# Kernel tuning notes

Measured on AMD Instinct MI355X. Metric: run time of the kernel, lower is better.

## Reference

```python
import jax, jax.numpy as jnp
import numpy as np

N_NODES = 50000
N_EDGES = 800000
N_REL = 3
N_GRAPHS = 500
EMB = 128
IN_DIM = EMB * 3
HID = 256
N_CLASS = 10
N_SHAPE, N_COLOR, MAX_POS = 8, 8, 128


def rgcn_layer(h, src, dst, etype, W, root, b):
    """PyG RGCNConv with default aggr='mean':
    out[v] = sum_r mean_{(j->v) in E_r} h[j] @ W[r] + h[v] @ root + b
    Aggregate raw features per (dst, relation) bucket, then apply relation matmuls.
    """
    N, R = h.shape[0], W.shape[0]
    seg = dst * R + etype  # combined (node, relation) segment id
    sums = jax.ops.segment_sum(h[src], seg, num_segments=N * R)          # (N*R, d)
    cnt = jax.ops.segment_sum(jnp.ones(seg.shape, h.dtype), seg, num_segments=N * R)
    mean = (sums / jnp.maximum(cnt, 1.0)[:, None]).reshape(N, R, -1)     # (N, R, d)
    return jnp.einsum('nrd,rdh->nh', mean, W) + h @ root + b


def setup_inputs() -> dict:
    key = jax.random.key(0)
    ks = jax.random.split(key, 20)
    f32 = jnp.float32
    inp = {
        's': jax.random.randint(ks[0], (N_NODES,), 0, N_SHAPE),
        'c': jax.random.randint(ks[1], (N_NODES,), 0, N_COLOR),
        'p': jax.random.randint(ks[2], (N_NODES,), 0, MAX_POS),
        'edge_index': jax.random.randint(ks[3], (2, N_EDGES), 0, N_NODES),
        'edge_type': jax.random.randint(ks[4], (N_EDGES,), 0, N_REL),
        'batch': jnp.sort(jax.random.randint(ks[5], (N_NODES,), 0, N_GRAPHS)),
        'shape_emb': jax.random.normal(ks[6], (N_SHAPE, EMB), f32),
        'color_emb': jax.random.normal(ks[7], (N_COLOR, EMB), f32),
        'pos_emb': jax.random.normal(ks[8], (MAX_POS, EMB), f32),
        'W1': jax.random.normal(ks[9], (N_REL, IN_DIM, HID), f32) / np.sqrt(IN_DIM),
        'root1': jax.random.normal(ks[10], (IN_DIM, HID), f32) / np.sqrt(IN_DIM),
        'b1': jnp.zeros((HID,), f32),
        'W2': jax.random.normal(ks[11], (N_REL, HID, HID), f32) / np.sqrt(HID),
        'root2': jax.random.normal(ks[12], (HID, HID), f32) / np.sqrt(HID),
        'b2': jnp.zeros((HID,), f32),
        'lin_w': jax.random.normal(ks[13], (HID, N_CLASS), f32) / np.sqrt(HID),
        'lin_b': jnp.zeros((N_CLASS,), f32),
    }
    return inp


def reference(s, c, p, edge_index, edge_type, batch,
              shape_emb, color_emb, pos_emb,
              W1, root1, b1, W2, root2, b2, lin_w, lin_b):
    src, dst = edge_index[0], edge_index[1]
    h = jnp.concatenate([shape_emb[s], color_emb[c], pos_emb[p]], axis=-1)  # (N, 3*emb)
    h = jax.nn.relu(rgcn_layer(h, src, dst, edge_type, W1, root1, b1))
    h = jax.nn.relu(rgcn_layer(h, src, dst, edge_type, W2, root2, b2))
    # global_mean_pool over graphs
    gsum = jax.ops.segment_sum(h, batch, num_segments=N_GRAPHS)
    gcnt = jax.ops.segment_sum(jnp.ones((h.shape[0],), h.dtype), batch, num_segments=N_GRAPHS)
    pooled = gsum / jnp.maximum(gcnt, 1.0)[:, None]
    return pooled @ lin_w + lin_b
```

## Files before the change

### kernel.cpp

```cpp
#include <hip/hip_runtime.h>
#include <hip/hip_bf16.h>

#define NN 50000
#define NE 800000
#define NR 3
#define NG 500
#define NB (NN * NR)
#define NCLS 10
#define NCMB 8192
#define CHUNK 2048
#define NBLK ((NB + CHUNK - 1) / CHUNK)

typedef __hip_bfloat16 bf16;
typedef __attribute__((ext_vector_type(8))) short short8;
typedef __attribute__((ext_vector_type(4))) float floatx4;

static __device__ __forceinline__ float b2f(bf16 x) { return __bfloat162float(x); }
static __device__ __forceinline__ bf16  f2b(float x) { return __float2bfloat16(x); }
static __device__ __forceinline__ float bs2f(short x) {
    return __bfloat162float(*reinterpret_cast<const bf16*>(&x));
}
static __device__ __forceinline__ short f2bs(float x) {
    bf16 b = __float2bfloat16(x);
    return *reinterpret_cast<const short*>(&b);
}

__global__ __launch_bounds__(256) void zero_u32(unsigned* __restrict__ p, long n) {
    long i = (long)blockIdx.x * 256 + threadIdx.x;
    if (i < n) p[i] = 0u;
}

__global__ __launch_bounds__(256) void count_edges(const int* __restrict__ ei,
                                                   const int* __restrict__ et,
                                                   int* __restrict__ cnt) {
    int e = blockIdx.x * 256 + threadIdx.x;
    if (e >= NE) return;
    atomicAdd(&cnt[ei[NE + e] * NR + et[e]], 1);
}

__global__ __launch_bounds__(256) void scan_block_sums(const int* __restrict__ cnt,
                                                       int* __restrict__ bsum) {
    __shared__ int sm[256];
    int b = blockIdx.x, t = threadIdx.x;
    int base = b * CHUNK + t * 8, s = 0;
#pragma unroll
    for (int j = 0; j < 8; ++j) { int i = base + j; if (i < NB) s += cnt[i]; }
    sm[t] = s; __syncthreads();
    for (int st = 128; st; st >>= 1) { if (t < st) sm[t] += sm[t + st]; __syncthreads(); }
    if (!t) bsum[b] = sm[0];
}

__global__ void scan_base(const int* __restrict__ bsum, int* __restrict__ bbase,
                          int* __restrict__ off) {
    if (threadIdx.x == 0 && blockIdx.x == 0) {
        int run = 0;
        for (int i = 0; i < NBLK; ++i) { bbase[i] = run; run += bsum[i]; }
        off[NB] = run;
    }
}

__global__ __launch_bounds__(256) void scan_write(const int* __restrict__ cnt,
                                                  const int* __restrict__ bbase,
                                                  int* __restrict__ off,
                                                  int* __restrict__ cursor) {
    int b = blockIdx.x, t = threadIdx.x;
    int base = b * CHUNK + t * 8;
    int v[8], ts = 0;
#pragma unroll
    for (int j = 0; j < 8; ++j) { int i = base + j; v[j] = (i < NB) ? cnt[i] : 0; ts += v[j]; }
    int lane = t & 63, wv = t >> 6;
    int incl = ts;
    for (int d = 1; d < 64; d <<= 1) {
        int o = __shfl_up(incl, d, 64);
        if (lane >= d) incl += o;
    }
    __shared__ int wsum[4];
    if (lane == 63) wsum[wv] = incl;
    __syncthreads();
    int wbase = 0;
    for (int w = 0; w < wv; ++w) wbase += wsum[w];
    int run = bbase[b] + wbase + incl - ts;
#pragma unroll
    for (int j = 0; j < 8; ++j) {
        int i = base + j;
        if (i < NB) { off[i] = run; cursor[i] = run; }
        run += v[j];
    }
}

__global__ __launch_bounds__(256) void scatter_edges(const int* __restrict__ ei,
                                                     const int* __restrict__ et,
                                                     const int* __restrict__ combo,
                                                     int* __restrict__ cursor,
                                                     int* __restrict__ eidx,
                                                     int* __restrict__ ecmb) {
    int e = blockIdx.x * 256 + threadIdx.x;
    if (e >= NE) return;
    int b = ei[NE + e] * NR + et[e];
    int pos = atomicAdd(&cursor[b], 1);
    int s = ei[e];
    eidx[pos] = s;
    ecmb[pos] = combo[s];
}

__global__ __launch_bounds__(256) void tab_gemm(const float* __restrict__ se,
                                                const float* __restrict__ ce,
                                                const float* __restrict__ pe,
                                                const float* __restrict__ W1,
                                                const float* __restrict__ root1,
                                                float* __restrict__ tab) {
    int bid = blockIdx.x;
    int r = bid / 144, row = bid % 144;
    int t = threadIdx.x;
    const float* A; int segk;
    if (row < 8)       { A = se + row * 128;        segk = 0; }
    else if (row < 16) { A = ce + (row - 8) * 128;  segk = 128; }
    else               { A = pe + (row - 16) * 128; segk = 256; }
    const float* W = (r < 3) ? (W1 + (size_t)r * 384 * 256) : root1;
    float acc = 0.f;
    for (int k = 0; k < 128; ++k)
        acc += A[k] * W[(size_t)(segk + k) * 256 + t];
    tab[((size_t)r * 144 + row) * 256 + t] = acc;
}

__global__ __launch_bounds__(256) void node_combo(const int* __restrict__ s,
                                                  const int* __restrict__ c,
                                                  const int* __restrict__ p,
                                                  int* __restrict__ combo) {
    int n = blockIdx.x * 256 + threadIdx.x;
    if (n < NN) combo[n] = (s[n] << 10) | (c[n] << 7) | p[n];
}

__global__ __launch_bounds__(256) void comb_build(const float* __restrict__ tab,
                                                  const float* __restrict__ b1,
                                                  bf16* __restrict__ comb) {
    int bid = blockIdx.x;
    int r = bid >> 13, cmb = bid & (NCMB - 1);
    int d = threadIdx.x;
    int si = cmb >> 10, ci = (cmb >> 7) & 7, pi = cmb & 127;
    const float* tr = tab + (size_t)r * 144 * 256;
    float v = tr[si * 256 + d] + tr[(8 + ci) * 256 + d] + tr[(16 + pi) * 256 + d];
    if (r == 3) v += b1[d];
    comb[(size_t)bid * 256 + d] = f2b(v);
}

__global__ __launch_bounds__(256) void l1_fused(const int* __restrict__ off,
                                                const int* __restrict__ ecmb,
                                                const int* __restrict__ combo,
                                                const bf16* __restrict__ comb,
                                                bf16* __restrict__ h1) {
    int wave = threadIdx.x >> 6, lane = threadIdx.x & 63;
    int dst = blockIdx.x * 4 + wave;
    if (dst >= NN) return;
    int half = lane >> 5, li8 = (lane & 31) * 8;
    float acc[8];
    if (half == 0) {
        int cmbD = combo[dst];
        short8 rv = *(const short8*)(comb + ((size_t)(3 * NCMB) + cmbD) * 256 + li8);
#pragma unroll
        for (int i = 0; i < 8; ++i) acc[i] = bs2f(rv[i]);
    } else {
#pragma unroll
        for (int i = 0; i < 8; ++i) acc[i] = 0.f;
    }
    for (int r = 0; r < NR; ++r) {
        int lo = off[dst * NR + r], hi = off[dst * NR + r + 1];
        if (hi <= lo) continue;
        const bf16* cr = comb + (size_t)r * NCMB * 256;
        float s[8] = {};
        int j = lo;
        for (; j + 8 <= hi; j += 8) {
            int c0 = ecmb[j + half],     c1 = ecmb[j + 2 + half];
            int c2 = ecmb[j + 4 + half], c3 = ecmb[j + 6 + half];
            short8 v0 = *(const short8*)(cr + (size_t)c0 * 256 + li8);
            short8 v1 = *(const short8*)(cr + (size_t)c1 * 256 + li8);
            short8 v2 = *(const short8*)(cr + (size_t)c2 * 256 + li8);
            short8 v3 = *(const short8*)(cr + (size_t)c3 * 256 + li8);
#pragma unroll
            for (int i = 0; i < 8; ++i)
                s[i] += (bs2f(v0[i]) + bs2f(v1[i])) + (bs2f(v2[i]) + bs2f(v3[i]));
        }
        for (; j + 2 <= hi; j += 2) {
            int c0 = ecmb[j + half];
            short8 v0 = *(const short8*)(cr + (size_t)c0 * 256 + li8);
#pragma unroll
            for (int i = 0; i < 8; ++i) s[i] += bs2f(v0[i]);
        }
        if (j < hi && half == 0) {
            short8 v0 = *(const short8*)(cr + (size_t)ecmb[j] * 256 + li8);
#pragma unroll
            for (int i = 0; i < 8; ++i) s[i] += bs2f(v0[i]);
        }
        float inv = 1.0f / (float)(hi - lo);
#pragma unroll
        for (int i = 0; i < 8; ++i) {
            float tot = s[i] + __shfl_xor(s[i], 32);
            if (half == 0) acc[i] += tot * inv;
        }
    }
    if (half == 0) {
        short8 o;
#pragma unroll
        for (int i = 0; i < 8; ++i) o[i] = f2bs(fmaxf(acc[i], 0.f));
        *(short8*)(h1 + (size_t)dst * 256 + li8) = o;
    }
}

__global__ __launch_bounds__(256) void agg_all(const int* __restrict__ off,
                                               const int* __restrict__ eidx,
                                               const bf16* __restrict__ h1,
                                               bf16* __restrict__ hagg) {
    int wave = threadIdx.x >> 6, lane = threadIdx.x & 63;
    int dst = blockIdx.x * 4 + wave;
    if (dst >= NN) return;
    int half = lane >> 5, li8 = (lane & 31) * 8;
    for (int r = 0; r < NR; ++r) {
        int lo = off[dst * NR + r], hi = off[dst * NR + r + 1];
        float s[8] = {};
        int j = lo;
        for (; j + 8 <= hi; j += 8) {
            int e0 = eidx[j + half],     e1 = eidx[j + 2 + half];
            int e2 = eidx[j + 4 + half], e3 = eidx[j + 6 + half];
            short8 v0 = *(const short8*)(h1 + (size_t)e0 * 256 + li8);
            short8 v1 = *(const short8*)(h1 + (size_t)e1 * 256 + li8);
            short8 v2 = *(const short8*)(h1 + (size_t)e2 * 256 + li8);
            short8 v3 = *(const short8*)(h1 + (size_t)e3 * 256 + li8);
#pragma unroll
            for (int i = 0; i < 8; ++i)
                s[i] += (bs2f(v0[i]) + bs2f(v1[i])) + (bs2f(v2[i]) + bs2f(v3[i]));
        }
        for (; j + 2 <= hi; j += 2) {
            int e0 = eidx[j + half];
            short8 v0 = *(const short8*)(h1 + (size_t)e0 * 256 + li8);
#pragma unroll
            for (int i = 0; i < 8; ++i) s[i] += bs2f(v0[i]);
        }
        if (j < hi && half == 0) {
            short8 v0 = *(const short8*)(h1 + (size_t)eidx[j] * 256 + li8);
#pragma unroll
            for (int i = 0; i < 8; ++i) s[i] += bs2f(v0[i]);
        }
        float inv = (hi > lo) ? 1.0f / (float)(hi - lo) : 0.f;
        short8 o;
#pragma unroll
        for (int i = 0; i < 8; ++i) {
            float tot = s[i] + __shfl_xor(s[i], 32);
            o[i] = f2bs(tot * inv);
        }
        if (half == 0)
            *(short8*)(hagg + (size_t)dst * 768 + r * 256 + li8) = o;
    }
}

__global__ __launch_bounds__(256) void conv_w2cat(const float* __restrict__ W2,
                                                  const float* __restrict__ root2,
                                                  bf16* __restrict__ Wf) {
    int idx = blockIdx.x * 256 + threadIdx.x;
    if (idx >= 256 * 1024) return;
    int j     = idx & 7;
    int lane  = (idx >> 3) & 63;
    int ni    = (idx >> 9) & 3;
    int chunk = (idx >> 11) & 31;
    int colblk = idx >> 16;
    int col = colblk * 64 + ni * 16 + (lane & 15);
    int k   = chunk * 32 + (lane >> 4) * 8 + j;
    float v = (k < 768) ? W2[((size_t)(k >> 8) * 256 + (k & 255)) * 256 + col]
                        : root2[(size_t)(k - 768) * 256 + col];
    Wf[idx] = f2b(v);
}

__global__ __launch_bounds__(256) void gemm_cat(const bf16* __restrict__ hagg,
                                                const bf16* __restrict__ h1,
                                                const bf16* __restrict__ Wf,
                                                const float* __restrict__ bias,
                                                bf16* __restrict__ h2) {
    __shared__ short lds[4][32 * 40];
    const int t = threadIdx.x;
    const int wave = t >> 6, lane = t & 63;
    const int quad = lane >> 4, l16 = lane & 15;
    const int row0 = blockIdx.y * 64 + (wave & 1) * 32;
    const int colblk = blockIdx.x * 2 + (wave >> 1);
    const int rsub = lane >> 2;
    const int ksub = (lane & 3) * 8;
    short* A = lds[wave];

    const int r0 = min(row0 + rsub, NN - 1);
    const int r1 = min(row0 + 16 + rsub, NN - 1);
    const bf16* gA0 = hagg + (size_t)r0 * 768 + ksub;
    const bf16* gA1 = hagg + (size_t)r1 * 768 + ksub;
    const bf16* gH0 = h1 + (size_t)r0 * 256 + ksub;
    const bf16* gH1 = h1 + (size_t)r1 * 256 + ksub;
    const short8* bbase = (const short8*)Wf + (size_t)colblk * 32 * 4 * 64 + lane;

    auto loadA2 = [&](int k0, short8& a0, short8& a1) {
        if (k0 < 768) { a0 = *(const short8*)(gA0 + k0); a1 = *(const short8*)(gA1 + k0); }
        else          { a0 = *(const short8*)(gH0 + k0 - 768); a1 = *(const short8*)(gH1 + k0 - 768); }
    };
    auto loadB = [&](int chunk, short8* bf4) {
        const short8* bp = bbase + (size_t)chunk * 4 * 64;
#pragma unroll
        for (int ni = 0; ni < 4; ++ni) bf4[ni] = bp[ni * 64];
    };

    floatx4 acc[2][4] = {};
    short8 aC0, aC1, bC[4], aN0, aN1, bN[4];
    loadA2(0, aC0, aC1);
    loadB(0, bC);

    for (int i = 0; i < 32; ++i) {
        *(short8*)&A[rsub * 40 + ksub] = aC0;
        *(short8*)&A[(16 + rsub) * 40 + ksub] = aC1;
        if (i + 1 < 32) {
            loadA2((i + 1) * 32, aN0, aN1);
            loadB(i + 1, bN);
        }
        short8 af0 = *(const short8*)&A[l16 * 40 + quad * 8];
        short8 af1 = *(const short8*)&A[(16 + l16) * 40 + quad * 8];
#pragma unroll
        for (int ni = 0; ni < 4; ++ni) {
            acc[0][ni] = __builtin_amdgcn_mfma_f32_16x16x32_bf16(af0, bC[ni], acc[0][ni], 0, 0, 0);
            acc[1][ni] = __builtin_amdgcn_mfma_f32_16x16x32_bf16(af1, bC[ni], acc[1][ni], 0, 0, 0);
        }
        aC0 = aN0; aC1 = aN1;
#pragma unroll
        for (int ni = 0; ni < 4; ++ni) bC[ni] = bN[ni];
    }

#pragma unroll
    for (int mi = 0; mi < 2; ++mi) {
#pragma unroll
        for (int ni = 0; ni < 4; ++ni) {
            int n = colblk * 64 + ni * 16 + l16;
            float bn = bias[n];
#pragma unroll
            for (int ii = 0; ii < 4; ++ii) {
                int gm = row0 + mi * 16 + quad * 4 + ii;
                if (gm < NN) {
                    float v = acc[mi][ni][ii] + bn;
                    h2[(size_t)gm * 256 + n] = f2b(fmaxf(v, 0.f));
                }
            }
        }
    }
}

#define PN 64
__global__ __launch_bounds__(256) void pool_rle(const int* __restrict__ batch,
                                                const bf16* __restrict__ H,
                                                float* __restrict__ pool,
                                                float* __restrict__ gcnt) {
    int t = threadIdx.x;
    int n0 = blockIdx.x * PN;
    int nend = n0 + PN; if (nend > NN) nend = NN;
    int curg = batch[n0];
    float acc = 0.f, cnt = 0.f;
    for (int n = n0; n < nend; ++n) {
        int g = batch[n];
        if (g != curg) {
            atomicAdd(&pool[(size_t)curg * 256 + t], acc);
            if (t == 0) atomicAdd(&gcnt[curg], cnt);
            acc = 0.f; cnt = 0.f; curg = g;
        }
        acc += b2f(H[(size_t)n * 256 + t]);
        cnt += 1.f;
    }
    atomicAdd(&pool[(size_t)curg * 256 + t], acc);
    if (t == 0) atomicAdd(&gcnt[curg], cnt);
}

__global__ __launch_bounds__(256) void final_head(const float* __restrict__ pool,
                                                  const float* __restrict__ gcnt,
                                                  const float* __restrict__ lin_w,
                                                  const float* __restrict__ lin_b,
                                                  float* __restrict__ out) {
    __shared__ float sm[256];
    int g = blockIdx.x, t = threadIdx.x;
    float inv = 1.0f / fmaxf(gcnt[g], 1.0f);
    sm[t] = pool[(size_t)g * 256 + t] * inv;
    __syncthreads();
    if (t < NCLS) {
        float s = lin_b[t];
        for (int d = 0; d < 256; ++d) s += sm[d] * lin_w[d * NCLS + t];
        out[g * NCLS + t] = s;
    }
}

extern "C" void kernel_launch(void* const* d_in, const int* in_sizes, int n_in,
                              void* d_out, int out_size, void* d_ws, size_t ws_size,
                              hipStream_t stream) {
    const int*   s_idx = (const int*)d_in[0];
    const int*   c_idx = (const int*)d_in[1];
    const int*   p_idx = (const int*)d_in[2];
    const int*   ei    = (const int*)d_in[3];
    const int*   et    = (const int*)d_in[4];
    const int*   batch = (const int*)d_in[5];
    const float* se    = (const float*)d_in[6];
    const float* ce    = (const float*)d_in[7];
    const float* pe    = (const float*)d_in[8];
    const float* W1    = (const float*)d_in[9];
    const float* root1 = (const float*)d_in[10];
    const float* b1    = (const float*)d_in[11];
    const float* W2    = (const float*)d_in[12];
    const float* root2 = (const float*)d_in[13];
    const float* b2    = (const float*)d_in[14];
    const float* lin_w = (const float*)d_in[15];
    const float* lin_b = (const float*)d_in[16];
    float* out = (float*)d_out;

    char* w = (char*)d_ws;
    size_t o = 0;
    auto alloc = [&](size_t bytes) -> void* {
        o = (o + 15) & ~(size_t)15;
        void* ptr = w + o;
        o += bytes;
        return ptr;
    };
    bf16*  hagg   = (bf16*) alloc((size_t)NN * 768 * 2);
    bf16*  h1     = (bf16*) alloc((size_t)NN * 256 * 2);
    bf16*  h2     = (bf16*) alloc((size_t)NN * 256 * 2);
    bf16*  comb   = (bf16*) alloc((size_t)4 * NCMB * 256 * 2);
    int*   combo  = (int*)  alloc((size_t)NN * 4);
    int*   eidx   = (int*)  alloc((size_t)NE * 4);
    int*   ecmb   = (int*)  alloc((size_t)NE * 4);
    int*   cnt    = (int*)  alloc((size_t)NB * 4);
    int*   off    = (int*)  alloc((size_t)(NB + 1) * 4);
    int*   cursor = (int*)  alloc((size_t)NB * 4);
    int*   bsum   = (int*)  alloc((size_t)NBLK * 4);
    int*   bbase  = (int*)  alloc((size_t)NBLK * 4);
    float* tab    = (float*)alloc((size_t)4 * 144 * 256 * 4);
    bf16*  Wf     = (bf16*) alloc((size_t)256 * 1024 * 2);
    float* pool   = (float*)alloc((size_t)NG * 256 * 4);
    float* gcnt   = (float*)alloc((size_t)NG * 4);
    (void)ws_size;

    node_combo<<<(NN + 255) / 256, 256, 0, stream>>>(s_idx, c_idx, p_idx, combo);
    zero_u32<<<(NB + 255) / 256, 256, 0, stream>>>((unsigned*)cnt, NB);
    count_edges<<<(NE + 255) / 256, 256, 0, stream>>>(ei, et, cnt);
    scan_block_sums<<<NBLK, 256, 0, stream>>>(cnt, bsum);
    scan_base<<<1, 64, 0, stream>>>(bsum, bbase, off);
    scan_write<<<NBLK, 256, 0, stream>>>(cnt, bbase, off, cursor);
    scatter_edges<<<(NE + 255) / 256, 256, 0, stream>>>(ei, et, combo, cursor, eidx, ecmb);

    tab_gemm<<<4 * 144, 256, 0, stream>>>(se, ce, pe, W1, root1, tab);
    comb_build<<<4 * NCMB, 256, 0, stream>>>(tab, b1, comb);
    conv_w2cat<<<(256 * 1024 + 255) / 256, 256, 0, stream>>>(W2, root2, Wf);

    l1_fused<<<(NN + 3) / 4, 256, 0, stream>>>(off, ecmb, combo, comb, h1);

    agg_all<<<(NN + 3) / 4, 256, 0, stream>>>(off, eidx, h1, hagg);
    dim3 g2(2, (NN + 63) / 64);
    gemm_cat<<<g2, 256, 0, stream>>>(hagg, h1, Wf, b2, h2);

    zero_u32<<<(NG * 256 + NG + 255) / 256, 256, 0, stream>>>((unsigned*)pool, NG * 256 + NG);
    pool_rle<<<(NN + PN - 1) / PN, 256, 0, stream>>>(batch, h2, pool, gcnt);
    final_head<<<NG, 256, 0, stream>>>(pool, gcnt, lin_w, lin_b, out);
}
```

Before: 434.9 us.

## Merge prep kernels, fold scan base into scan_write, double-buffer gemm LDS

Independent setup kernels (combo, zeroing, table GEMM, W2 conversion) are merged into one launch, and the edge counting and comb table build into a second. The single-thread scan_base kernel is removed: each scan_write block now sums the preceding block totals itself. The gemm_cat main loop gets two LDS buffers and two register sets so global loads for the next step overlap the MFMAs on the current one. Together these cut launch count and serialization, at the cost of a small redundant prefix sum per block and higher register and LDS use in the GEMM.

```diff
diff --git a/kernel.cpp b/kernel.cpp
--- a/kernel.cpp
+++ b/kernel.cpp
@@ -11,6 +11,16 @@
 #define CHUNK 2048
 #define NBLK ((NB + CHUNK - 1) / CHUNK)
 
+#define P1_COMBO   196
+#define P1_ZCNT    586
+#define P1_ZPOOL   502
+#define P1_TAB     576
+#define P1_WF      1024
+#define P1_TOTAL   (P1_COMBO + P1_ZCNT + P1_ZPOOL + P1_TAB + P1_WF)
+#define P2_CNT     3125
+#define P2_COMB    (4 * NCMB)
+#define P2_TOTAL   (P2_CNT + P2_COMB)
+
 typedef __hip_bfloat16 bf16;
 typedef __attribute__((ext_vector_type(8))) short short8;
 typedef __attribute__((ext_vector_type(4))) float floatx4;
@@ -25,17 +35,90 @@
     return *reinterpret_cast<const short*>(&b);
 }
 
-__global__ __launch_bounds__(256) void zero_u32(unsigned* __restrict__ p, long n) {
-    long i = (long)blockIdx.x * 256 + threadIdx.x;
-    if (i < n) p[i] = 0u;
-}
-
-__global__ __launch_bounds__(256) void count_edges(const int* __restrict__ ei,
-                                                   const int* __restrict__ et,
-                                                   int* __restrict__ cnt) {
-    int e = blockIdx.x * 256 + threadIdx.x;
-    if (e >= NE) return;
-    atomicAdd(&cnt[ei[NE + e] * NR + et[e]], 1);
+__global__ __launch_bounds__(256) void prep1(const int* __restrict__ s,
+                                             const int* __restrict__ c,
+                                             const int* __restrict__ p,
+                                             const float* __restrict__ se,
+                                             const float* __restrict__ ce,
+                                             const float* __restrict__ pe,
+                                             const float* __restrict__ W1,
+                                             const float* __restrict__ root1,
+                                             const float* __restrict__ W2,
+                                             const float* __restrict__ root2,
+                                             int* __restrict__ combo,
+                                             unsigned* __restrict__ cnt,
+                                             unsigned* __restrict__ poolz,
+                                             float* __restrict__ tab,
+                                             bf16* __restrict__ Wf) {
+    int b = blockIdx.x, t = threadIdx.x;
+    if (b < P1_COMBO) {
+        int n = b * 256 + t;
+        if (n < NN) combo[n] = (s[n] << 10) | (c[n] << 7) | p[n];
+        return;
+    }
+    b -= P1_COMBO;
+    if (b < P1_ZCNT) {
+        int i = b * 256 + t;
+        if (i < NB) cnt[i] = 0u;
+        return;
+    }
+    b -= P1_ZCNT;
+    if (b < P1_ZPOOL) {
+        int i = b * 256 + t;
+        if (i < NG * 256 + NG) poolz[i] = 0u;
+        return;
+    }
+    b -= P1_ZPOOL;
+    if (b < P1_TAB) {
+        int r = b / 144, row = b % 144;
+        const float* A; int segk;
+        if (row < 8)       { A = se + row * 128;        segk = 0; }
+        else if (row < 16) { A = ce + (row - 8) * 128;  segk = 128; }
+        else               { A = pe + (row - 16) * 128; segk = 256; }
+        const float* W = (r < 3) ? (W1 + (size_t)r * 384 * 256) : root1;
+        float acc = 0.f;
+        for (int k = 0; k < 128; ++k)
+            acc += A[k] * W[(size_t)(segk + k) * 256 + t];
+        tab[((size_t)r * 144 + row) * 256 + t] = acc;
+        return;
+    }
+    b -= P1_TAB;
+    {
+        int idx = b * 256 + t;
+        int j     = idx & 7;
+        int lane  = (idx >> 3) & 63;
+        int ni    = (idx >> 9) & 3;
+        int chunk = (idx >> 11) & 31;
+        int colblk = idx >> 16;
+        int col = colblk * 64 + ni * 16 + (lane & 15);
+        int k   = chunk * 32 + (lane >> 4) * 8 + j;
+        float v = (k < 768) ? W2[((size_t)(k >> 8) * 256 + (k & 255)) * 256 + col]
+                            : root2[(size_t)(k - 768) * 256 + col];
+        Wf[idx] = f2b(v);
+    }
+}
+
+__global__ __launch_bounds__(256) void prep2(const int* __restrict__ ei,
+                                             const int* __restrict__ et,
+                                             int* __restrict__ cnt,
+                                             const float* __restrict__ tab,
+                                             const float* __restrict__ b1,
+                                             bf16* __restrict__ comb) {
+    int b = blockIdx.x, t = threadIdx.x;
+    if (b < P2_CNT) {
+        int e = b * 256 + t;
+        if (e < NE) atomicAdd(&cnt[ei[NE + e] * NR + et[e]], 1);
+        return;
+    }
+    b -= P2_CNT;
+    {
+        int r = b >> 13, cmb = b & (NCMB - 1);
+        int si = cmb >> 10, ci = (cmb >> 7) & 7, pi = cmb & 127;
+        const float* tr = tab + (size_t)r * 144 * 256;
+        float v = tr[si * 256 + t] + tr[(8 + ci) * 256 + t] + tr[(16 + pi) * 256 + t];
+        if (r == 3) v += b1[t];
+        comb[(size_t)b * 256 + t] = f2b(v);
+    }
 }
 
 __global__ __launch_bounds__(256) void scan_block_sums(const int* __restrict__ cnt,
@@ -50,20 +133,18 @@
     if (!t) bsum[b] = sm[0];
 }
 
-__global__ void scan_base(const int* __restrict__ bsum, int* __restrict__ bbase,
-                          int* __restrict__ off) {
-    if (threadIdx.x == 0 && blockIdx.x == 0) {
-        int run = 0;
-        for (int i = 0; i < NBLK; ++i) { bbase[i] = run; run += bsum[i]; }
-        off[NB] = run;
-    }
-}
-
 __global__ __launch_bounds__(256) void scan_write(const int* __restrict__ cnt,
-                                                  const int* __restrict__ bbase,
+                                                  const int* __restrict__ bsum,
                                                   int* __restrict__ off,
                                                   int* __restrict__ cursor) {
     int b = blockIdx.x, t = threadIdx.x;
+    int bbase = 0;
+    for (int i = 0; i < b; ++i) bbase += bsum[i];
+    if (b == 0 && t == 0) {
+        int tot = 0;
+        for (int i = 0; i < NBLK; ++i) tot += bsum[i];
+        off[NB] = tot;
+    }
     int base = b * CHUNK + t * 8;
     int v[8], ts = 0;
 #pragma unroll
@@ -79,7 +160,7 @@
     __syncthreads();
     int wbase = 0;
     for (int w = 0; w < wv; ++w) wbase += wsum[w];
-    int run = bbase[b] + wbase + incl - ts;
+    int run = bbase + wbase + incl - ts;
 #pragma unroll
     for (int j = 0; j < 8; ++j) {
         int i = base + j;
@@ -101,47 +182,6 @@
     int s = ei[e];
     eidx[pos] = s;
     ecmb[pos] = combo[s];
-}
-
-__global__ __launch_bounds__(256) void tab_gemm(const float* __restrict__ se,
-                                                const float* __restrict__ ce,
-                                                const float* __restrict__ pe,
-                                                const float* __restrict__ W1,
-                                                const float* __restrict__ root1,
-                                                float* __restrict__ tab) {
-    int bid = blockIdx.x;
-    int r = bid / 144, row = bid % 144;
-    int t = threadIdx.x;
-    const float* A; int segk;
-    if (row < 8)       { A = se + row * 128;        segk = 0; }
-    else if (row < 16) { A = ce + (row - 8) * 128;  segk = 128; }
-    else               { A = pe + (row - 16) * 128; segk = 256; }
-    const float* W = (r < 3) ? (W1 + (size_t)r * 384 * 256) : root1;
-    float acc = 0.f;
-    for (int k = 0; k < 128; ++k)
-        acc += A[k] * W[(size_t)(segk + k) * 256 + t];
-    tab[((size_t)r * 144 + row) * 256 + t] = acc;
-}
-
-__global__ __launch_bounds__(256) void node_combo(const int* __restrict__ s,
-                                                  const int* __restrict__ c,
-                                                  const int* __restrict__ p,
-                                                  int* __restrict__ combo) {
-    int n = blockIdx.x * 256 + threadIdx.x;
-    if (n < NN) combo[n] = (s[n] << 10) | (c[n] << 7) | p[n];
-}
-
-__global__ __launch_bounds__(256) void comb_build(const float* __restrict__ tab,
-                                                  const float* __restrict__ b1,
-                                                  bf16* __restrict__ comb) {
-    int bid = blockIdx.x;
-    int r = bid >> 13, cmb = bid & (NCMB - 1);
-    int d = threadIdx.x;
-    int si = cmb >> 10, ci = (cmb >> 7) & 7, pi = cmb & 127;
-    const float* tr = tab + (size_t)r * 144 * 256;
-    float v = tr[si * 256 + d] + tr[(8 + ci) * 256 + d] + tr[(16 + pi) * 256 + d];
-    if (r == 3) v += b1[d];
-    comb[(size_t)bid * 256 + d] = f2b(v);
 }
 
 __global__ __launch_bounds__(256) void l1_fused(const int* __restrict__ off,
@@ -252,29 +292,12 @@
     }
 }
 
-__global__ __launch_bounds__(256) void conv_w2cat(const float* __restrict__ W2,
-                                                  const float* __restrict__ root2,
-                                                  bf16* __restrict__ Wf) {
-    int idx = blockIdx.x * 256 + threadIdx.x;
-    if (idx >= 256 * 1024) return;
-    int j     = idx & 7;
-    int lane  = (idx >> 3) & 63;
-    int ni    = (idx >> 9) & 3;
-    int chunk = (idx >> 11) & 31;
-    int colblk = idx >> 16;
-    int col = colblk * 64 + ni * 16 + (lane & 15);
-    int k   = chunk * 32 + (lane >> 4) * 8 + j;
-    float v = (k < 768) ? W2[((size_t)(k >> 8) * 256 + (k & 255)) * 256 + col]
-                        : root2[(size_t)(k - 768) * 256 + col];
-    Wf[idx] = f2b(v);
-}
-
 __global__ __launch_bounds__(256) void gemm_cat(const bf16* __restrict__ hagg,
                                                 const bf16* __restrict__ h1,
                                                 const bf16* __restrict__ Wf,
                                                 const float* __restrict__ bias,
                                                 bf16* __restrict__ h2) {
-    __shared__ short lds[4][32 * 40];
+    __shared__ short lds[4][2][32 * 40];
     const int t = threadIdx.x;
     const int wave = t >> 6, lane = t & 63;
     const int quad = lane >> 4, l16 = lane & 15;
@@ -282,7 +305,8 @@
     const int colblk = blockIdx.x * 2 + (wave >> 1);
     const int rsub = lane >> 2;
     const int ksub = (lane & 3) * 8;
-    short* A = lds[wave];
+    short* A0 = lds[wave][0];
+    short* A1 = lds[wave][1];
 
     const int r0 = min(row0 + rsub, NN - 1);
     const int r1 = min(row0 + 16 + rsub, NN - 1);
@@ -303,27 +327,37 @@
     };
 
     floatx4 acc[2][4] = {};
-    short8 aC0, aC1, bC[4], aN0, aN1, bN[4];
-    loadA2(0, aC0, aC1);
-    loadB(0, bC);
-
-    for (int i = 0; i < 32; ++i) {
-        *(short8*)&A[rsub * 40 + ksub] = aC0;
-        *(short8*)&A[(16 + rsub) * 40 + ksub] = aC1;
-        if (i + 1 < 32) {
-            loadA2((i + 1) * 32, aN0, aN1);
-            loadB(i + 1, bN);
-        }
-        short8 af0 = *(const short8*)&A[l16 * 40 + quad * 8];
-        short8 af1 = *(const short8*)&A[(16 + l16) * 40 + quad * 8];
-#pragma unroll
-        for (int ni = 0; ni < 4; ++ni) {
-            acc[0][ni] = __builtin_amdgcn_mfma_f32_16x16x32_bf16(af0, bC[ni], acc[0][ni], 0, 0, 0);
-            acc[1][ni] = __builtin_amdgcn_mfma_f32_16x16x32_bf16(af1, bC[ni], acc[1][ni], 0, 0, 0);
-        }
-        aC0 = aN0; aC1 = aN1;
-#pragma unroll
-        for (int ni = 0; ni < 4; ++ni) bC[ni] = bN[ni];
+    short8 aE0, aE1, bE[4];
+    short8 aO0, aO1, bO[4];
+    loadA2(0, aE0, aE1);  loadB(0, bE);
+    loadA2(32, aO0, aO1); loadB(1, bO);
+
+#pragma unroll
+    for (int i = 0; i < 32; i += 2) {
+        *(short8*)&A0[rsub * 40 + ksub] = aE0;
+        *(short8*)&A0[(16 + rsub) * 40 + ksub] = aE1;
+        {
+            short8 af0 = *(const short8*)&A0[l16 * 40 + quad * 8];
+            short8 af1 = *(const short8*)&A0[(16 + l16) * 40 + quad * 8];
+#pragma unroll
+            for (int ni = 0; ni < 4; ++ni) {
+                acc[0][ni] = __builtin_amdgcn_mfma_f32_16x16x32_bf16(af0, bE[ni], acc[0][ni], 0, 0, 0);
+                acc[1][ni] = __builtin_amdgcn_mfma_f32_16x16x32_bf16(af1, bE[ni], acc[1][ni], 0, 0, 0);
+            }
+        }
+        if (i + 2 < 32) { loadA2((i + 2) * 32, aE0, aE1); loadB(i + 2, bE); }
+        *(short8*)&A1[rsub * 40 + ksub] = aO0;
+        *(short8*)&A1[(16 + rsub) * 40 + ksub] = aO1;
+        {
+            short8 af0 = *(const short8*)&A1[l16 * 40 + quad * 8];
+            short8 af1 = *(const short8*)&A1[(16 + l16) * 40 + quad * 8];
+#pragma unroll
+            for (int ni = 0; ni < 4; ++ni) {
+                acc[0][ni] = __builtin_amdgcn_mfma_f32_16x16x32_bf16(af0, bO[ni], acc[0][ni], 0, 0, 0);
+                acc[1][ni] = __builtin_amdgcn_mfma_f32_16x16x32_bf16(af1, bO[ni], acc[1][ni], 0, 0, 0);
+            }
+        }
+        if (i + 3 < 32) { loadA2((i + 3) * 32, aO0, aO1); loadB(i + 3, bO); }
     }
 
 #pragma unroll
@@ -426,32 +460,23 @@
     int*   off    = (int*)  alloc((size_t)(NB + 1) * 4);
     int*   cursor = (int*)  alloc((size_t)NB * 4);
     int*   bsum   = (int*)  alloc((size_t)NBLK * 4);
-    int*   bbase  = (int*)  alloc((size_t)NBLK * 4);
     float* tab    = (float*)alloc((size_t)4 * 144 * 256 * 4);
     bf16*  Wf     = (bf16*) alloc((size_t)256 * 1024 * 2);
     float* pool   = (float*)alloc((size_t)NG * 256 * 4);
     float* gcnt   = (float*)alloc((size_t)NG * 4);
     (void)ws_size;
 
-    node_combo<<<(NN + 255) / 256, 256, 0, stream>>>(s_idx, c_idx, p_idx, combo);
-    zero_u32<<<(NB + 255) / 256, 256, 0, stream>>>((unsigned*)cnt, NB);
-    count_edges<<<(NE + 255) / 256, 256, 0, stream>>>(ei, et, cnt);
+    prep1<<<P1_TOTAL, 256, 0, stream>>>(s_idx, c_idx, p_idx, se, ce, pe,
+                                        W1, root1, W2, root2,
+                                        combo, (unsigned*)cnt, (unsigned*)pool, tab, Wf);
+    prep2<<<P2_TOTAL, 256, 0, stream>>>(ei, et, cnt, tab, b1, comb);
     scan_block_sums<<<NBLK, 256, 0, stream>>>(cnt, bsum);
-    scan_base<<<1, 64, 0, stream>>>(bsum, bbase, off);
-    scan_write<<<NBLK, 256, 0, stream>>>(cnt, bbase, off, cursor);
+    scan_write<<<NBLK, 256, 0, stream>>>(cnt, bsum, off, cursor);
     scatter_edges<<<(NE + 255) / 256, 256, 0, stream>>>(ei, et, combo, cursor, eidx, ecmb);
-
-    tab_gemm<<<4 * 144, 256, 0, stream>>>(se, ce, pe, W1, root1, tab);
-    comb_build<<<4 * NCMB, 256, 0, stream>>>(tab, b1, comb);
-    conv_w2cat<<<(256 * 1024 + 255) / 256, 256, 0, stream>>>(W2, root2, Wf);
-
     l1_fused<<<(NN + 3) / 4, 256, 0, stream>>>(off, ecmb, combo, comb, h1);
-
     agg_all<<<(NN + 3) / 4, 256, 0, stream>>>(off, eidx, h1, hagg);
     dim3 g2(2, (NN + 63) / 64);
     gemm_cat<<<g2, 256, 0, stream>>>(hagg, h1, Wf, b2, h2);
-
-    zero_u32<<<(NG * 256 + NG + 255) / 256, 256, 0, stream>>>((unsigned*)pool, NG * 256 + NG);
     pool_rle<<<(NN + PN - 1) / PN, 256, 0, stream>>>(batch, h2, pool, gcnt);
     final_head<<<NG, 256, 0, stream>>>(pool, gcnt, lin_w, lin_b, out);
 }
```

After: 424.6 us. 2.4% less time.
